# Kernel tuning notes

Hardware: AMD Instinct MI355X
Metric: run time of the kernel (lower is better)

The kernel has to match this reference:

```python
import jax, jax.numpy as jnp
import numpy as np

DIM = 96
D_STATE = 16
EXPAND = 2
D_INNER = EXPAND * DIM
DT_RANK = (DIM + 15) // 16  # 6
B, H, W = 2, 64, 64
K = 4  # scan directions


def _ln(x, w, b, eps=1e-5):
    mu = x.mean(-1, keepdims=True)
    var = x.var(-1, keepdims=True)
    return (x - mu) / jnp.sqrt(var + eps) * w + b


def setup_inputs() -> dict:
    key = jax.random.key(0)
    ks = jax.random.split(key, 10)
    f = jnp.float32
    x = jax.random.normal(ks[0], (B, H, W, DIM), dtype=f)
    y = jax.random.normal(ks[1], (B, H, W, DIM), dtype=f)
    inp = {
        'x': x,
        'y': y,
        'ln_w': jnp.ones((DIM,), f),
        'ln_b': jnp.zeros((DIM,), f),
        'in_proj_w': jax.random.normal(ks[2], (2 * D_INNER, DIM), f) * 0.05,
        'conv_w': jax.random.normal(ks[3], (D_INNER, 1, 3, 3), f) * 0.1,
        'conv_b': jnp.zeros((D_INNER,), f),
        'x_proj_w': jax.random.normal(ks[4], (K, DT_RANK + 2 * D_STATE, D_INNER), f) * 0.05,
        'dt_w': jax.random.normal(ks[5], (K, D_INNER, DT_RANK), f) * 0.1,
        'dt_b': jax.random.normal(ks[6], (K, D_INNER), f) * 0.1,
        'A_log': jnp.broadcast_to(jnp.log(jnp.arange(1, D_STATE + 1, dtype=f)), (K, D_INNER, D_STATE)),
        'Ds': jnp.ones((K, D_INNER), f),
        'out_norm_w': jnp.ones((D_INNER,), f),
        'out_norm_b': jnp.zeros((D_INNER,), f),
        'out_proj_w': jax.random.normal(ks[7], (DIM, D_INNER), f) * 0.05,
    }
    return inp


def _fwd(x, y, ln_w, ln_b, in_proj_w, conv_w, conv_b, x_proj_w, dt_w, dt_b,
         A_log, Ds, out_norm_w, out_norm_b, out_proj_w):
    Bsz, Hh, Ww, C = x.shape
    Din = conv_w.shape[0]
    N = A_log.shape[-1]
    R = dt_w.shape[-1]
    L = Hh * Ww

    diff = jnp.abs(x - y)                       # TemporalSpectrumBlock abs-diff
    h = _ln(diff, ln_w, ln_b)                   # VSSBlock ln_1
    xz = h @ in_proj_w.T                        # (B,H,W,2*Din)
    xm, z = jnp.split(xz, 2, axis=-1)
    xm = xm.transpose(0, 3, 1, 2)               # (B,Din,H,W)
    xm = jax.lax.conv_general_dilated(
        xm, conv_w, (1, 1), 'SAME', feature_group_count=Din,
        dimension_numbers=('NCHW', 'OIHW', 'NCHW')) + conv_b[None, :, None, None]
    xm = jax.nn.silu(xm)

    # 4-directional sequences (B,4,Din,L)
    x0 = xm.reshape(Bsz, Din, L)
    x1 = xm.transpose(0, 1, 3, 2).reshape(Bsz, Din, L)
    xs = jnp.stack([x0, x1], axis=1)
    xs = jnp.concatenate([xs, jnp.flip(xs, axis=-1)], axis=1)

    x_dbl = jnp.einsum('bkdl,kcd->bkcl', xs, x_proj_w)
    dts, Bs, Cs = jnp.split(x_dbl, [R, R + N], axis=2)   # (B,4,R,L),(B,4,N,L),(B,4,N,L)
    dts = jnp.einsum('bkrl,kdr->bkdl', dts, dt_w)
    delta = jax.nn.softplus(dts + dt_b[None, :, :, None])  # (B,4,Din,L)

    A = -jnp.exp(A_log)                                    # (4,Din,N)
    dA = jnp.exp(delta[..., None] * A[None, :, :, None, :])          # (B,4,Din,L,N)
    dBu = delta[..., None] * Bs.transpose(0, 1, 3, 2)[:, :, None] * xs[..., None]

    dA_t = dA.transpose(3, 0, 1, 2, 4)    # (L,B,4,Din,N)
    dBu_t = dBu.transpose(3, 0, 1, 2, 4)
    C_t = Cs.transpose(3, 0, 1, 2)        # (L,B,4,N)
    h0 = jnp.zeros((Bsz, 4, Din, N), dtype=x.dtype)

    def step(hc, inp):
        a, bu, c = inp
        hc = a * hc + bu
        yv = jnp.einsum('bkdn,bkn->bkd', hc, c)
        return hc, yv

    _, ys = jax.lax.scan(step, h0, (dA_t, dBu_t, C_t))    # (L,B,4,Din)
    ys = ys.transpose(1, 2, 3, 0)                          # (B,4,Din,L)
    out_y = ys + Ds[None, :, :, None] * xs

    inv_y = jnp.flip(out_y[:, 2:4], axis=-1)
    wh_y = out_y[:, 1].reshape(Bsz, Din, Ww, Hh).transpose(0, 1, 3, 2).reshape(Bsz, Din, L)
    invwh_y = inv_y[:, 1].reshape(Bsz, Din, Ww, Hh).transpose(0, 1, 3, 2).reshape(Bsz, Din, L)
    yc = out_y[:, 0] + inv_y[:, 0] + wh_y + invwh_y        # (B,Din,L)
    yc = yc.transpose(0, 2, 1).reshape(Bsz, Hh, Ww, Din)

    yn = _ln(yc, out_norm_w, out_norm_b)
    out = (yn * jax.nn.silu(z)) @ out_proj_w.T
    return diff + out                                      # residual around the block


def reference(x, y, ln_w, ln_b, in_proj_w, conv_w, conv_b, x_proj_w, dt_w, dt_b,
              A_log, Ds, out_norm_w, out_norm_b, out_proj_w):
    return _fwd(x, y, ln_w, ln_b, in_proj_w, conv_w, conv_b, x_proj_w, dt_w, dt_b,
                A_log, Ds, out_norm_w, out_norm_b, out_proj_w)
```

## Files before the change

kernel.cpp:

```cpp
#include <hip/hip_runtime.h>
#include <math.h>

#define DIMC 96
#define DIN  192
#define NST  16
#define RNK  6
#define KD   4
#define HH   64
#define WWD  64
#define LL   4096
#define BB   2
#define NC   128
#define CH   32
#define CPK  48

__device__ __forceinline__ int pos_of(int k, int l) {
    int t = ((l & 63) << 6) | (l >> 6);
    switch (k) {
        case 0: return l;
        case 1: return t;
        case 2: return LL - 1 - l;
        default: return ((((LL-1-l) & 63) << 6) | ((LL-1-l) >> 6));
    }
}

__device__ __forceinline__ float silu_f(float v) {
    return v / (1.f + __expf(-v));
}

__global__ __launch_bounds__(256) void k0_prep(
    const float* __restrict__ Win, const float* __restrict__ Wout,
    const float* __restrict__ xpw,
    float* __restrict__ WinT, float* __restrict__ WoutT, float* __restrict__ wT3)
{
    int idx = blockIdx.x*256 + threadIdx.x;
    int stride = gridDim.x*256;
    for (int i = idx; i < 96*384; i += stride) {
        int j = i / 384, o = i - j*384;
        WinT[i] = Win[o*96 + j];
    }
    for (int i = idx; i < 192*96; i += stride) {
        int j = i / 96, o = i - j*96;
        WoutT[i] = Wout[o*192 + j];
    }
    for (int i = idx; i < KD*192*CPK; i += stride) {
        int kk = i / (192*CPK); int rem = i - kk*192*CPK;
        int j = rem / CPK, c = rem - j*CPK;
        float v = 0.f;
        if (c < 16)       v = xpw[((size_t)kk*(RNK+2*NST) + RNK + c)*DIN + j];
        else if (c < 32)  v = xpw[((size_t)kk*(RNK+2*NST) + RNK + NST + (c-16))*DIN + j];
        else if (c < 38)  v = xpw[((size_t)kk*(RNK+2*NST) + (c-32))*DIN + j];
        wT3[i] = v;
    }
}

__global__ __launch_bounds__(1024) void k1_ln_inproj(
    const float* __restrict__ x, const float* __restrict__ y,
    const float* __restrict__ lnw, const float* __restrict__ lnb,
    const float* __restrict__ WinT,
    float* __restrict__ diff, float* __restrict__ xm, float* __restrict__ zbuf)
{
    __shared__ float hT[96*65];
    __shared__ float ps1[16*64], ps2[16*64];
    __shared__ float mus[64], rss[64];
    int t = threadIdx.x;
    int ptile = blockIdx.x >> 1, cgrp = blockIdx.x & 1;
    int p0 = ptile*64;

    #pragma unroll
    for (int s = 0; s < 6; s++) {
        int i = t + 1024*s;
        float v = fabsf(x[(size_t)p0*96 + i] - y[(size_t)p0*96 + i]);
        if (cgrp == 0) diff[(size_t)p0*96 + i] = v;
        int pos = i / 96, ch = i - pos*96;
        hT[ch*65 + pos] = v;
    }
    __syncthreads();
    {
        int pos = t & 63, part = t >> 6;
        float s1 = 0.f, s2 = 0.f;
        #pragma unroll
        for (int m = 0; m < 6; m++) {
            float v = hT[(part*6 + m)*65 + pos];
            s1 += v; s2 += v*v;
        }
        ps1[part*64 + pos] = s1; ps2[part*64 + pos] = s2;
    }
    __syncthreads();
    if (t < 64) {
        float S1 = 0.f, S2 = 0.f;
        #pragma unroll
        for (int i = 0; i < 16; i++) { S1 += ps1[i*64 + t]; S2 += ps2[i*64 + t]; }
        float mu = S1 * (1.f/96.f);
        float var = S2 * (1.f/96.f) - mu*mu;
        mus[t] = mu; rss[t] = rsqrtf(var + 1e-5f);
    }
    __syncthreads();
    #pragma unroll
    for (int s = 0; s < 6; s++) {
        int i = t + 1024*s;
        int pos = i / 96, ch = i - pos*96;
        hT[ch*65 + pos] = (hT[ch*65 + pos] - mus[pos]) * rss[pos] * lnw[ch] + lnb[ch];
    }
    __syncthreads();

    int w = __builtin_amdgcn_readfirstlane(t >> 6);
    int lane = t & 63;
    int c0 = cgrp*192 + w*12;
    const float* wp = WinT + c0;
    float acc[12];
    #pragma unroll
    for (int cc = 0; cc < 12; cc++) acc[cc] = 0.f;
    #pragma unroll 2
    for (int j = 0; j < 96; j++) {
        float u = hT[j*65 + lane];
        const float* wrow = wp + j*384;
        #pragma unroll
        for (int cc = 0; cc < 12; cc++) acc[cc] += u * wrow[cc];
    }
    size_t p = (size_t)(p0 + lane);
    float* dst = (c0 < 192) ? (xm + p*192 + c0) : (zbuf + p*192 + (c0 - 192));
    #pragma unroll
    for (int q = 0; q < 3; q++)
        *(float4*)&dst[4*q] = make_float4(acc[4*q], acc[4*q+1], acc[4*q+2], acc[4*q+3]);
}

__global__ __launch_bounds__(192) void k2_conv(
    const float* __restrict__ xm, const float* __restrict__ cw,
    const float* __restrict__ cb, float* __restrict__ xconv)
{
    int p = blockIdx.x;
    int d = threadIdx.x;
    int b = p >> 12;
    int l = p & (LL - 1);
    int hh = l >> 6, ww = l & 63;
    float acc = cb[d];
    const float* wd = cw + d*9;
    #pragma unroll
    for (int di = -1; di <= 1; di++) {
        int h2 = hh + di;
        if ((unsigned)h2 < HH) {
            #pragma unroll
            for (int dj = -1; dj <= 1; dj++) {
                int w2 = ww + dj;
                if ((unsigned)w2 < WWD)
                    acc += wd[(di+1)*3 + (dj+1)] * xm[((size_t)b*LL + h2*WWD + w2)*DIN + d];
            }
        }
    }
    xconv[(size_t)p*DIN + d] = silu_f(acc);
}

__global__ __launch_bounds__(512) void k3_xproj(
    const float* __restrict__ xconv, const float* __restrict__ wT3,
    float* __restrict__ XDK)
{
    __shared__ float uT[192*65];
    int t = threadIdx.x;
    int ptile = blockIdx.x >> 1, wgrp = blockIdx.x & 1;
    int p0 = ptile*64;

    #pragma unroll
    for (int s = 0; s < 24; s++) {
        int i = t + 512*s;
        int pos = i / 192, ch = i - pos*192;
        uT[ch*65 + pos] = xconv[(size_t)(p0 + pos)*192 + ch];
    }
    __syncthreads();

    int w = __builtin_amdgcn_readfirstlane(t >> 6);
    int slot = wgrp*8 + w;
    int k = slot >> 2, cq = slot & 3;
    int lane = t & 63;
    int c0 = cq*12;
    const float* wp = wT3 + (size_t)k*192*CPK + c0;
    float acc[12];
    #pragma unroll
    for (int cc = 0; cc < 12; cc++) acc[cc] = 0.f;
    #pragma unroll 2
    for (int j = 0; j < 192; j++) {
        float u = uT[j*65 + lane];
        const float* wrow = wp + j*CPK;
        #pragma unroll
        for (int cc = 0; cc < 12; cc++) acc[cc] += u * wrow[cc];
    }
    int p = p0 + lane;
    int b = p >> 12;
    int s = p & (LL - 1);
    int ts = ((s & 63) << 6) | (s >> 6);
    int l;
    switch (k) {
        case 0: l = s; break;
        case 1: l = ts; break;
        case 2: l = LL - 1 - s; break;
        default: l = LL - 1 - ts; break;
    }
    float* dst = XDK + ((size_t)(b*KD + k)*LL + l)*CPK + c0;
    #pragma unroll
    for (int q = 0; q < 3; q++)
        *(float4*)&dst[4*q] = make_float4(acc[4*q], acc[4*q+1], acc[4*q+2], acc[4*q+3]);
}

__global__ __launch_bounds__(192) void k4_scanA(
    const float* __restrict__ xconv, const float* __restrict__ XDK,
    const float* __restrict__ dtw, const float* __restrict__ dtb,
    const float* __restrict__ A_log,
    float* __restrict__ Sarr, float* __restrict__ Q)
{
    int blk = blockIdx.x;
    int c  = blk & (NC - 1);
    int bk = blk >> 7;
    int k  = bk & 3;
    int b  = bk >> 2;
    int d  = threadIdx.x;
    float dw[RNK];
    #pragma unroll
    for (int r = 0; r < RNK; r++) dw[r] = dtw[((size_t)k*DIN + d)*RNK + r];
    float bias = dtb[k*DIN + d];
    float A[NST];
    #pragma unroll
    for (int n = 0; n < NST; n++) A[n] = -__expf(A_log[((size_t)k*DIN + d)*NST + n]);
    bool fastA = true;
    #pragma unroll
    for (int n = 1; n < NST; n++)
        fastA = fastA && (fabsf(A[n] - (float)(n+1)*A[0]) <= 1e-4f*(float)(n+1));

    float h[NST];
    #pragma unroll
    for (int n = 0; n < NST; n++) h[n] = 0.f;
    float S = 0.f;

    size_t rb = ((size_t)bk*LL + c*CH)*CPK;
    if (fastA) {
        #pragma unroll 2
        for (int step = 0; step < CH; step++) {
            const float* rec = XDK + rb + step*CPK;
            float dl = bias;
            #pragma unroll
            for (int r = 0; r < RNK; r++) dl += rec[32 + r] * dw[r];
            dl = (dl > 20.f) ? dl : __logf(1.f + __expf(dl));
            int l = c*CH + step;
            float uu = xconv[((size_t)b*LL + pos_of(k, l))*DIN + d];
            float du = dl * uu;
            S += dl;
            float e1 = __expf(dl * A[0]);
            float e2 = e1*e1, e4 = e2*e2;
            float p0 = e1, p1 = e2, p2 = e2*e1, p3 = e4;
            #pragma unroll
            for (int g = 0; g < 4; g++) {
                h[4*g+0] = p0*h[4*g+0] + du*rec[4*g+0];
                h[4*g+1] = p1*h[4*g+1] + du*rec[4*g+1];
                h[4*g+2] = p2*h[4*g+2] + du*rec[4*g+2];
                h[4*g+3] = p3*h[4*g+3] + du*rec[4*g+3];
                if (g < 3) { p0 *= e4; p1 *= e4; p2 *= e4; p3 *= e4; }
            }
        }
    } else {
        #pragma unroll 2
        for (int step = 0; step < CH; step++) {
            const float* rec = XDK + rb + step*CPK;
            float dl = bias;
            #pragma unroll
            for (int r = 0; r < RNK; r++) dl += rec[32 + r] * dw[r];
            dl = (dl > 20.f) ? dl : __logf(1.f + __expf(dl));
            int l = c*CH + step;
            float uu = xconv[((size_t)b*LL + pos_of(k, l))*DIN + d];
            float du = dl * uu;
            S += dl;
            #pragma unroll
            for (int n = 0; n < NST; n++) {
                float a = __expf(dl * A[n]);
                h[n] = a*h[n] + du*rec[n];
            }
        }
    }
    Sarr[(size_t)blk*DIN + d] = S;
    size_t qb = (size_t)blk*NST*DIN + d;
    #pragma unroll
    for (int n = 0; n < NST; n++) Q[qb + n*DIN] = h[n];
}

__global__ __launch_bounds__(256) void k5_scanB(
    const float* __restrict__ A_log, const float* __restrict__ Sarr,
    float* __restrict__ Q)
{
    int idx = blockIdx.x*256 + threadIdx.x;
    if (idx >= BB*KD*NST*DIN) return;
    int d = idx % DIN;
    int rest = idx / DIN;
    int n = rest % NST; rest /= NST;
    int k = rest & 3;
    int b = rest >> 2;
    int bk = b*KD + k;
    float A = -__expf(A_log[((size_t)k*DIN + d)*NST + n]);
    size_t qstride = (size_t)NST*DIN;
    size_t qbase = (size_t)bk*NC*qstride + n*DIN + d;
    size_t sbase = (size_t)bk*NC*DIN + d;
    float h = 0.f;
    #pragma unroll 4
    for (int c = 0; c < NC; c++) {
        float s = Sarr[sbase + c*DIN];
        float q = Q[qbase + c*qstride];
        Q[qbase + c*qstride] = h;
        h = __expf(A*s)*h + q;
    }
}

__global__ __launch_bounds__(192) void k6_scanC(
    const float* __restrict__ xconv, const float* __restrict__ XDK,
    const float* __restrict__ dtw, const float* __restrict__ dtb,
    const float* __restrict__ A_log, const float* __restrict__ Ds,
    const float* __restrict__ Q, float* __restrict__ outy)
{
    int blk = blockIdx.x;
    int c  = blk & (NC - 1);
    int bk = blk >> 7;
    int k  = bk & 3;
    int b  = bk >> 2;
    int d  = threadIdx.x;
    float dw[RNK];
    #pragma unroll
    for (int r = 0; r < RNK; r++) dw[r] = dtw[((size_t)k*DIN + d)*RNK + r];
    float bias = dtb[k*DIN + d];
    float A[NST];
    #pragma unroll
    for (int n = 0; n < NST; n++) A[n] = -__expf(A_log[((size_t)k*DIN + d)*NST + n]);
    bool fastA = true;
    #pragma unroll
    for (int n = 1; n < NST; n++)
        fastA = fastA && (fabsf(A[n] - (float)(n+1)*A[0]) <= 1e-4f*(float)(n+1));
    float h[NST];
    size_t qb = (size_t)blk*NST*DIN + d;
    #pragma unroll
    for (int n = 0; n < NST; n++) h[n] = Q[qb + n*DIN];
    float Dv = Ds[k*DIN + d];

    size_t rb = ((size_t)bk*LL + c*CH)*CPK;
    if (fastA) {
        #pragma unroll 2
        for (int step = 0; step < CH; step++) {
            const float* rec = XDK + rb + step*CPK;
            float dl = bias;
            #pragma unroll
            for (int r = 0; r < RNK; r++) dl += rec[32 + r] * dw[r];
            dl = (dl > 20.f) ? dl : __logf(1.f + __expf(dl));
            int l = c*CH + step;
            int sp = pos_of(k, l);
            float uu = xconv[((size_t)b*LL + sp)*DIN + d];
            float du = dl * uu;
            float e1 = __expf(dl * A[0]);
            float e2 = e1*e1, e4 = e2*e2;
            float p0 = e1, p1 = e2, p2 = e2*e1, p3 = e4;
            float yv = 0.f;
            #pragma unroll
            for (int g = 0; g < 4; g++) {
                h[4*g+0] = p0*h[4*g+0] + du*rec[4*g+0];
                h[4*g+1] = p1*h[4*g+1] + du*rec[4*g+1];
                h[4*g+2] = p2*h[4*g+2] + du*rec[4*g+2];
                h[4*g+3] = p3*h[4*g+3] + du*rec[4*g+3];
                yv += h[4*g+0]*rec[16+4*g+0] + h[4*g+1]*rec[16+4*g+1]
                    + h[4*g+2]*rec[16+4*g+2] + h[4*g+3]*rec[16+4*g+3];
                if (g < 3) { p0 *= e4; p1 *= e4; p2 *= e4; p3 *= e4; }
            }
            outy[((size_t)bk*LL + sp)*DIN + d] = yv + Dv*uu;
        }
    } else {
        #pragma unroll 2
        for (int step = 0; step < CH; step++) {
            const float* rec = XDK + rb + step*CPK;
            float dl = bias;
            #pragma unroll
            for (int r = 0; r < RNK; r++) dl += rec[32 + r] * dw[r];
            dl = (dl > 20.f) ? dl : __logf(1.f + __expf(dl));
            int l = c*CH + step;
            int sp = pos_of(k, l);
            float uu = xconv[((size_t)b*LL + sp)*DIN + d];
            float du = dl * uu;
            float yv = 0.f;
            #pragma unroll
            for (int n = 0; n < NST; n++) {
                float a = __expf(dl * A[n]);
                h[n] = a*h[n] + du*rec[n];
                yv += h[n] * rec[16 + n];
            }
            outy[((size_t)bk*LL + sp)*DIN + d] = yv + Dv*uu;
        }
    }
}

__global__ __launch_bounds__(256) void k7_out(
    const float* __restrict__ outy, const float* __restrict__ zbuf,
    const float* __restrict__ diff, const float* __restrict__ onw,
    const float* __restrict__ onb, const float* __restrict__ WoutT,
    float* __restrict__ out)
{
    __shared__ float gT[192*65];
    __shared__ float ps1[4*64], ps2[4*64];
    __shared__ float mus[64], rss[64];
    int t = threadIdx.x;
    int ptile = blockIdx.x >> 1, chalf = blockIdx.x & 1;
    int p0 = ptile*64;
    int b = p0 >> 12;
    int l0 = p0 & (LL - 1);
    const size_t seg = (size_t)LL*DIN;
    size_t base = ((size_t)(b*KD)*LL + l0)*DIN;

    #pragma unroll
    for (int s = 0; s < 48; s++) {
        int i = t + 256*s;
        float yc = outy[base + i] + outy[base + seg + i]
                 + outy[base + 2*seg + i] + outy[base + 3*seg + i];
        int pos = i / 192, ch = i - pos*192;
        gT[ch*65 + pos] = yc;
    }
    __syncthreads();
    {
        int pos = t & 63, part = t >> 6;
        float s1 = 0.f, s2 = 0.f;
        #pragma unroll
        for (int m = 0; m < 48; m++) {
            float v = gT[(part*48 + m)*65 + pos];
            s1 += v; s2 += v*v;
        }
        ps1[part*64 + pos] = s1; ps2[part*64 + pos] = s2;
    }
    __syncthreads();
    if (t < 64) {
        float S1 = ps1[t] + ps1[64+t] + ps1[128+t] + ps1[192+t];
        float S2 = ps2[t] + ps2[64+t] + ps2[128+t] + ps2[192+t];
        float mu = S1 * (1.f/192.f);
        float var = S2 * (1.f/192.f) - mu*mu;
        mus[t] = mu; rss[t] = rsqrtf(var + 1e-5f);
    }
    __syncthreads();
    #pragma unroll
    for (int s = 0; s < 48; s++) {
        int i = t + 256*s;
        int pos = i / 192, ch = i - pos*192;
        float v = gT[ch*65 + pos];
        float yn = (v - mus[pos]) * rss[pos] * onw[ch] + onb[ch];
        float z = zbuf[(size_t)p0*DIN + i];
        gT[ch*65 + pos] = yn * silu_f(z);
    }
    __syncthreads();

    int w = __builtin_amdgcn_readfirstlane(t >> 6);
    int lane = t & 63;
    int c0 = chalf*48 + w*12;
    const float* wp = WoutT + c0;
    float acc[12];
    #pragma unroll
    for (int cc = 0; cc < 12; cc++) acc[cc] = 0.f;
    #pragma unroll 2
    for (int j = 0; j < 192; j++) {
        float u = gT[j*65 + lane];
        const float* wrow = wp + j*96;
        #pragma unroll
        for (int cc = 0; cc < 12; cc++) acc[cc] += u * wrow[cc];
    }
    size_t p = (size_t)(p0 + lane);
    #pragma unroll
    for (int q = 0; q < 3; q++) {
        float4 dv = *(const float4*)&diff[p*96 + c0 + 4*q];
        *(float4*)&out[p*96 + c0 + 4*q] =
            make_float4(acc[4*q] + dv.x, acc[4*q+1] + dv.y, acc[4*q+2] + dv.z, acc[4*q+3] + dv.w);
    }
}

extern "C" void kernel_launch(void* const* d_in, const int* in_sizes, int n_in,
                              void* d_out, int out_size, void* d_ws, size_t ws_size,
                              hipStream_t stream)
{
    const float* x       = (const float*)d_in[0];
    const float* y       = (const float*)d_in[1];
    const float* ln_w    = (const float*)d_in[2];
    const float* ln_b    = (const float*)d_in[3];
    const float* in_proj = (const float*)d_in[4];
    const float* conv_w  = (const float*)d_in[5];
    const float* conv_b  = (const float*)d_in[6];
    const float* x_proj  = (const float*)d_in[7];
    const float* dt_w    = (const float*)d_in[8];
    const float* dt_b    = (const float*)d_in[9];
    const float* A_log   = (const float*)d_in[10];
    const float* Ds      = (const float*)d_in[11];
    const float* onw     = (const float*)d_in[12];
    const float* onb     = (const float*)d_in[13];
    const float* out_w   = (const float*)d_in[14];
    float* out = (float*)d_out;

    float* ws    = (float*)d_ws;
    float* diff  = ws;
    float* zbuf  = diff  + 786432;
    float* xm    = zbuf  + 1572864;
    float* xconv = xm    + 1572864;
    float* XDK   = xconv + 1572864;
    float* outy  = XDK   + 1572864;
    float* Qbuf  = outy  + 6291456;
    float* Sarr  = Qbuf  + 6291456;
    float* WinT  = Sarr  + 393216;
    float* WoutT = WinT  + 36864;
    float* wT3   = WoutT + 18432;

    const int BL = BB * LL;

    hipLaunchKernelGGL(k0_prep, dim3(144), dim3(256), 0, stream,
                       in_proj, out_w, x_proj, WinT, WoutT, wT3);
    hipLaunchKernelGGL(k1_ln_inproj, dim3(BL/64*2), dim3(1024), 0, stream,
                       x, y, ln_w, ln_b, WinT, diff, xm, zbuf);
    hipLaunchKernelGGL(k2_conv, dim3(BL), dim3(DIN), 0, stream,
                       xm, conv_w, conv_b, xconv);
    hipLaunchKernelGGL(k3_xproj, dim3(BL/64*2), dim3(512), 0, stream,
                       xconv, wT3, XDK);
    hipLaunchKernelGGL(k4_scanA, dim3(BB*KD*NC), dim3(DIN), 0, stream,
                       xconv, XDK, dt_w, dt_b, A_log, Sarr, Qbuf);
    hipLaunchKernelGGL(k5_scanB, dim3((BB*KD*NST*DIN + 255)/256), dim3(256), 0, stream,
                       A_log, Sarr, Qbuf);
    hipLaunchKernelGGL(k6_scanC, dim3(BB*KD*NC), dim3(DIN), 0, stream,
                       xconv, XDK, dt_w, dt_b, A_log, Ds, Qbuf, outy);
    hipLaunchKernelGGL(k7_out, dim3(BL/64*2), dim3(256), 0, stream,
                       outy, zbuf, diff, onw, onb, WoutT, out);
}
```

Baseline: 266.3 us.

## Add transposed xconv copy for scans and split output stage into two kernels

```diff
diff --git a/kernel.cpp b/kernel.cpp
--- a/kernel.cpp
+++ b/kernel.cpp
@@ -127,7 +127,8 @@
 
 __global__ __launch_bounds__(192) void k2_conv(
     const float* __restrict__ xm, const float* __restrict__ cw,
-    const float* __restrict__ cb, float* __restrict__ xconv)
+    const float* __restrict__ cb, float* __restrict__ xconv,
+    float* __restrict__ xconvT)
 {
     int p = blockIdx.x;
     int d = threadIdx.x;
@@ -148,7 +149,10 @@
             }
         }
     }
-    xconv[(size_t)p*DIN + d] = silu_f(acc);
+    float v = silu_f(acc);
+    xconv[(size_t)p*DIN + d] = v;
+    int tl = ((l & 63) << 6) | (l >> 6);
+    xconvT[((size_t)b*LL + tl)*DIN + d] = v;
 }
 
 __global__ __launch_bounds__(512) void k3_xproj(
@@ -202,7 +206,8 @@
 }
 
 __global__ __launch_bounds__(192) void k4_scanA(
-    const float* __restrict__ xconv, const float* __restrict__ XDK,
+    const float* __restrict__ xconv, const float* __restrict__ xconvT,
+    const float* __restrict__ XDK,
     const float* __restrict__ dtw, const float* __restrict__ dtb,
     const float* __restrict__ A_log,
     float* __restrict__ Sarr, float* __restrict__ Q)
@@ -213,6 +218,7 @@
     int k  = bk & 3;
     int b  = bk >> 2;
     int d  = threadIdx.x;
+    const float* xc = (k & 1) ? xconvT : xconv;
     float dw[RNK];
     #pragma unroll
     for (int r = 0; r < RNK; r++) dw[r] = dtw[((size_t)k*DIN + d)*RNK + r];
@@ -230,17 +236,18 @@
     for (int n = 0; n < NST; n++) h[n] = 0.f;
     float S = 0.f;
 
-    size_t rb = ((size_t)bk*LL + c*CH)*CPK;
+    size_t rb = ((size_t)bk*LL + c*CH);
     if (fastA) {
-        #pragma unroll 2
+        #pragma unroll 4
         for (int step = 0; step < CH; step++) {
-            const float* rec = XDK + rb + step*CPK;
+            const float* rec = XDK + (rb + step)*CPK;
             float dl = bias;
             #pragma unroll
             for (int r = 0; r < RNK; r++) dl += rec[32 + r] * dw[r];
             dl = (dl > 20.f) ? dl : __logf(1.f + __expf(dl));
             int l = c*CH + step;
-            float uu = xconv[((size_t)b*LL + pos_of(k, l))*DIN + d];
+            int li = (k < 2) ? l : (LL - 1 - l);
+            float uu = xc[((size_t)b*LL + li)*DIN + d];
             float du = dl * uu;
             S += dl;
             float e1 = __expf(dl * A[0]);
@@ -258,13 +265,14 @@
     } else {
         #pragma unroll 2
         for (int step = 0; step < CH; step++) {
-            const float* rec = XDK + rb + step*CPK;
+            const float* rec = XDK + (rb + step)*CPK;
             float dl = bias;
             #pragma unroll
             for (int r = 0; r < RNK; r++) dl += rec[32 + r] * dw[r];
             dl = (dl > 20.f) ? dl : __logf(1.f + __expf(dl));
             int l = c*CH + step;
-            float uu = xconv[((size_t)b*LL + pos_of(k, l))*DIN + d];
+            int li = (k < 2) ? l : (LL - 1 - l);
+            float uu = xc[((size_t)b*LL + li)*DIN + d];
             float du = dl * uu;
             S += dl;
             #pragma unroll
@@ -307,7 +315,8 @@
 }
 
 __global__ __launch_bounds__(192) void k6_scanC(
-    const float* __restrict__ xconv, const float* __restrict__ XDK,
+    const float* __restrict__ xconv, const float* __restrict__ xconvT,
+    const float* __restrict__ XDK,
     const float* __restrict__ dtw, const float* __restrict__ dtb,
     const float* __restrict__ A_log, const float* __restrict__ Ds,
     const float* __restrict__ Q, float* __restrict__ outy)
@@ -318,6 +327,7 @@
     int k  = bk & 3;
     int b  = bk >> 2;
     int d  = threadIdx.x;
+    const float* xc = (k & 1) ? xconvT : xconv;
     float dw[RNK];
     #pragma unroll
     for (int r = 0; r < RNK; r++) dw[r] = dtw[((size_t)k*DIN + d)*RNK + r];
@@ -335,18 +345,19 @@
     for (int n = 0; n < NST; n++) h[n] = Q[qb + n*DIN];
     float Dv = Ds[k*DIN + d];
 
-    size_t rb = ((size_t)bk*LL + c*CH)*CPK;
+    size_t rb = ((size_t)bk*LL + c*CH);
     if (fastA) {
-        #pragma unroll 2
+        #pragma unroll 4
         for (int step = 0; step < CH; step++) {
-            const float* rec = XDK + rb + step*CPK;
+            const float* rec = XDK + (rb + step)*CPK;
             float dl = bias;
             #pragma unroll
             for (int r = 0; r < RNK; r++) dl += rec[32 + r] * dw[r];
             dl = (dl > 20.f) ? dl : __logf(1.f + __expf(dl));
             int l = c*CH + step;
+            int li = (k < 2) ? l : (LL - 1 - l);
+            float uu = xc[((size_t)b*LL + li)*DIN + d];
             int sp = pos_of(k, l);
-            float uu = xconv[((size_t)b*LL + sp)*DIN + d];
             float du = dl * uu;
             float e1 = __expf(dl * A[0]);
             float e2 = e1*e1, e4 = e2*e2;
@@ -367,14 +378,15 @@
     } else {
         #pragma unroll 2
         for (int step = 0; step < CH; step++) {
-            const float* rec = XDK + rb + step*CPK;
+            const float* rec = XDK + (rb + step)*CPK;
             float dl = bias;
             #pragma unroll
             for (int r = 0; r < RNK; r++) dl += rec[32 + r] * dw[r];
             dl = (dl > 20.f) ? dl : __logf(1.f + __expf(dl));
             int l = c*CH + step;
+            int li = (k < 2) ? l : (LL - 1 - l);
+            float uu = xc[((size_t)b*LL + li)*DIN + d];
             int sp = pos_of(k, l);
-            float uu = xconv[((size_t)b*LL + sp)*DIN + d];
             float du = dl * uu;
             float yv = 0.f;
             #pragma unroll
@@ -388,82 +400,78 @@
     }
 }
 
-__global__ __launch_bounds__(256) void k7_out(
+__global__ __launch_bounds__(192) void k7a_comb(
     const float* __restrict__ outy, const float* __restrict__ zbuf,
-    const float* __restrict__ diff, const float* __restrict__ onw,
-    const float* __restrict__ onb, const float* __restrict__ WoutT,
-    float* __restrict__ out)
-{
-    __shared__ float gT[192*65];
-    __shared__ float ps1[4*64], ps2[4*64];
-    __shared__ float mus[64], rss[64];
-    int t = threadIdx.x;
-    int ptile = blockIdx.x >> 1, chalf = blockIdx.x & 1;
-    int p0 = ptile*64;
-    int b = p0 >> 12;
-    int l0 = p0 & (LL - 1);
+    const float* __restrict__ onw, const float* __restrict__ onb,
+    float* __restrict__ gbuf)
+{
+    __shared__ float red1[3], red2[3];
+    __shared__ float s_mu, s_rs;
+    int p = blockIdx.x;
+    int d = threadIdx.x;
+    int b = p >> 12;
     const size_t seg = (size_t)LL*DIN;
-    size_t base = ((size_t)(b*KD)*LL + l0)*DIN;
-
-    #pragma unroll
-    for (int s = 0; s < 48; s++) {
-        int i = t + 256*s;
-        float yc = outy[base + i] + outy[base + seg + i]
-                 + outy[base + 2*seg + i] + outy[base + 3*seg + i];
-        int pos = i / 192, ch = i - pos*192;
-        gT[ch*65 + pos] = yc;
-    }
-    __syncthreads();
-    {
-        int pos = t & 63, part = t >> 6;
-        float s1 = 0.f, s2 = 0.f;
-        #pragma unroll
-        for (int m = 0; m < 48; m++) {
-            float v = gT[(part*48 + m)*65 + pos];
-            s1 += v; s2 += v*v;
-        }
-        ps1[part*64 + pos] = s1; ps2[part*64 + pos] = s2;
-    }
-    __syncthreads();
-    if (t < 64) {
-        float S1 = ps1[t] + ps1[64+t] + ps1[128+t] + ps1[192+t];
-        float S2 = ps2[t] + ps2[64+t] + ps2[128+t] + ps2[192+t];
+    size_t base = ((size_t)(b*KD)*LL + (p & (LL-1)))*DIN + d;
+
+    float yc = outy[base] + outy[base + seg] + outy[base + 2*seg] + outy[base + 3*seg];
+
+    float s1 = yc, s2 = yc*yc;
+    #pragma unroll
+    for (int off = 32; off > 0; off >>= 1) {
+        s1 += __shfl_down(s1, off);
+        s2 += __shfl_down(s2, off);
+    }
+    int wid = d >> 6, lane = d & 63;
+    if (lane == 0) { red1[wid] = s1; red2[wid] = s2; }
+    __syncthreads();
+    if (d == 0) {
+        float S1 = red1[0] + red1[1] + red1[2];
+        float S2 = red2[0] + red2[1] + red2[2];
         float mu = S1 * (1.f/192.f);
         float var = S2 * (1.f/192.f) - mu*mu;
-        mus[t] = mu; rss[t] = rsqrtf(var + 1e-5f);
-    }
-    __syncthreads();
+        s_mu = mu; s_rs = rsqrtf(var + 1e-5f);
+    }
+    __syncthreads();
+    float yn = (yc - s_mu) * s_rs * onw[d] + onb[d];
+    gbuf[(size_t)p*DIN + d] = yn * silu_f(zbuf[(size_t)p*DIN + d]);
+}
+
+__global__ __launch_bounds__(256) void k7b_gemm(
+    const float* __restrict__ gbuf, const float* __restrict__ diff,
+    const float* __restrict__ WoutT, float* __restrict__ out)
+{
+    __shared__ float gT[192*65];
+    int t = threadIdx.x;
+    int ptile = blockIdx.x >> 2, cq = blockIdx.x & 3;
+    int p0 = ptile*64;
+
     #pragma unroll
     for (int s = 0; s < 48; s++) {
         int i = t + 256*s;
         int pos = i / 192, ch = i - pos*192;
-        float v = gT[ch*65 + pos];
-        float yn = (v - mus[pos]) * rss[pos] * onw[ch] + onb[ch];
-        float z = zbuf[(size_t)p0*DIN + i];
-        gT[ch*65 + pos] = yn * silu_f(z);
+        gT[ch*65 + pos] = gbuf[(size_t)(p0 + pos)*192 + ch];
     }
     __syncthreads();
 
     int w = __builtin_amdgcn_readfirstlane(t >> 6);
     int lane = t & 63;
-    int c0 = chalf*48 + w*12;
+    int c0 = cq*24 + w*6;
     const float* wp = WoutT + c0;
-    float acc[12];
-    #pragma unroll
-    for (int cc = 0; cc < 12; cc++) acc[cc] = 0.f;
+    float acc[6];
+    #pragma unroll
+    for (int cc = 0; cc < 6; cc++) acc[cc] = 0.f;
     #pragma unroll 2
     for (int j = 0; j < 192; j++) {
         float u = gT[j*65 + lane];
         const float* wrow = wp + j*96;
         #pragma unroll
-        for (int cc = 0; cc < 12; cc++) acc[cc] += u * wrow[cc];
+        for (int cc = 0; cc < 6; cc++) acc[cc] += u * wrow[cc];
     }
     size_t p = (size_t)(p0 + lane);
     #pragma unroll
     for (int q = 0; q < 3; q++) {
-        float4 dv = *(const float4*)&diff[p*96 + c0 + 4*q];
-        *(float4*)&out[p*96 + c0 + 4*q] =
-            make_float4(acc[4*q] + dv.x, acc[4*q+1] + dv.y, acc[4*q+2] + dv.z, acc[4*q+3] + dv.w);
+        float2 dv = *(const float2*)&diff[p*96 + c0 + 2*q];
+        *(float2*)&out[p*96 + c0 + 2*q] = make_float2(acc[2*q] + dv.x, acc[2*q+1] + dv.y);
     }
 }
 
@@ -488,18 +496,20 @@
     const float* out_w   = (const float*)d_in[14];
     float* out = (float*)d_out;
 
-    float* ws    = (float*)d_ws;
-    float* diff  = ws;
-    float* zbuf  = diff  + 786432;
-    float* xm    = zbuf  + 1572864;
-    float* xconv = xm    + 1572864;
-    float* XDK   = xconv + 1572864;
-    float* outy  = XDK   + 1572864;
-    float* Qbuf  = outy  + 6291456;
-    float* Sarr  = Qbuf  + 6291456;
-    float* WinT  = Sarr  + 393216;
-    float* WoutT = WinT  + 36864;
-    float* wT3   = WoutT + 18432;
+    float* ws     = (float*)d_ws;
+    float* diff   = ws;
+    float* zbuf   = diff   + 786432;
+    float* xm     = zbuf   + 1572864;
+    float* xconv  = xm     + 1572864;
+    float* xconvT = xconv  + 1572864;
+    float* XDK    = xconvT + 1572864;
+    float* outy   = XDK    + 1572864;
+    float* Qbuf   = outy   + 6291456;
+    float* Sarr   = Qbuf   + 3145728;
+    float* gbuf   = Sarr   + 196608;
+    float* WinT   = gbuf   + 1572864;
+    float* WoutT  = WinT   + 36864;
+    float* wT3    = WoutT  + 18432;
 
     const int BL = BB * LL;
 
@@ -508,15 +518,17 @@
     hipLaunchKernelGGL(k1_ln_inproj, dim3(BL/64*2), dim3(1024), 0, stream,
                        x, y, ln_w, ln_b, WinT, diff, xm, zbuf);
     hipLaunchKernelGGL(k2_conv, dim3(BL), dim3(DIN), 0, stream,
-                       xm, conv_w, conv_b, xconv);
+                       xm, conv_w, conv_b, xconv, xconvT);
     hipLaunchKernelGGL(k3_xproj, dim3(BL/64*2), dim3(512), 0, stream,
                        xconv, wT3, XDK);
     hipLaunchKernelGGL(k4_scanA, dim3(BB*KD*NC), dim3(DIN), 0, stream,
-                       xconv, XDK, dt_w, dt_b, A_log, Sarr, Qbuf);
+                       xconv, xconvT, XDK, dt_w, dt_b, A_log, Sarr, Qbuf);
     hipLaunchKernelGGL(k5_scanB, dim3((BB*KD*NST*DIN + 255)/256), dim3(256), 0, stream,
                        A_log, Sarr, Qbuf);
     hipLaunchKernelGGL(k6_scanC, dim3(BB*KD*NC), dim3(DIN), 0, stream,
-                       xconv, XDK, dt_w, dt_b, A_log, Ds, Qbuf, outy);
-    hipLaunchKernelGGL(k7_out, dim3(BL/64*2), dim3(256), 0, stream,
-                       outy, zbuf, diff, onw, onb, WoutT, out);
-}
+                       xconv, xconvT, XDK, dt_w, dt_b, A_log, Ds, Qbuf, outy);
+    hipLaunchKernelGGL(k7a_comb, dim3(BL), dim3(DIN), 0, stream,
+                       outy, zbuf, onw, onb, gbuf);
+    hipLaunchKernelGGL(k7b_gemm, dim3(128*4), dim3(256), 0, stream,
+                       gbuf, diff, WoutT, out);
+}
```

Result: slower. 273.6 us (+2.8%).
